# Optimization experiments

Hardware: AMD Instinct MI355X
Metric: run time of the kernel (lower is better)

## Reference

```python
import jax, jax.numpy as jnp
import numpy as np

GEMMA2_TANH_SCALE = 50.0
N_HEADS = 16
HEAD_DIM = 128
NEG_INF = -1e9


def setup_inputs() -> dict:
    key = jax.random.key(0)
    ks = jax.random.split(key, 5)
    B, S, D = 2, 2048, 2048
    H, HD = N_HEADS, HEAD_DIM
    x = jax.random.normal(ks[0], (B, S, D), jnp.float32)
    w_scale = 1.0 / np.sqrt(D)
    wq = jax.random.normal(ks[1], (H * HD, D), jnp.float32) * w_scale
    wk = jax.random.normal(ks[2], (H * HD, D), jnp.float32) * w_scale
    wv = jax.random.normal(ks[3], (H * HD, D), jnp.float32) * w_scale
    wo = jax.random.normal(ks[4], (D, H * HD), jnp.float32) * w_scale
    # RoPE frequencies: standard llama theta=10000, [S, HD/2, (cos,sin)]
    inv_freq = 1.0 / (10000.0 ** (np.arange(0, HD, 2, dtype=np.float32) / HD))
    ang = np.outer(np.arange(S, dtype=np.float32), inv_freq)  # [S, HD/2]
    freqs_cis = jnp.asarray(np.stack([np.cos(ang), np.sin(ang)], axis=-1), jnp.float32)
    # causal additive mask [1,1,S,S]
    causal = np.tril(np.ones((S, S), dtype=bool))
    mask = jnp.asarray(np.where(causal, 0.0, NEG_INF).astype(np.float32))[None, None]
    return {"x": x, "freqs_cis": freqs_cis, "mask": mask,
            "wq": wq, "wk": wk, "wv": wv, "wo": wo}


def _apply_rope(t, freqs_cis):
    # t: [B,S,H,HD]; treat adjacent pairs as complex, multiply by e^{i*ang}
    B, S, H, HD = t.shape
    tr = t.reshape(B, S, H, HD // 2, 2)
    a, b = tr[..., 0], tr[..., 1]
    cos = freqs_cis[None, :, None, :, 0]
    sin = freqs_cis[None, :, None, :, 1]
    out = jnp.stack([a * cos - b * sin, a * sin + b * cos], axis=-1)
    return out.reshape(B, S, H, HD)


def reference(x, freqs_cis, mask, wq, wk, wv, wo):
    B, S, D = x.shape
    H, HD = N_HEADS, HEAD_DIM
    xq = (x @ wq.T).reshape(B, S, H, HD)
    xk = (x @ wk.T).reshape(B, S, H, HD)
    xv = (x @ wv.T).reshape(B, S, H, HD)
    q = _apply_rope(xq, freqs_cis).transpose(0, 2, 1, 3)  # [B,H,S,HD]
    k = _apply_rope(xk, freqs_cis).transpose(0, 2, 1, 3)
    v = xv.transpose(0, 2, 1, 3)
    scores = jnp.einsum('bhqd,bhkd->bhqk', q, k) / np.sqrt(HD).astype(np.float32)
    # gemma2 tanh softcap
    scores = jnp.tanh(scores / GEMMA2_TANH_SCALE) * GEMMA2_TANH_SCALE
    scores = scores + mask
    probs = jax.nn.softmax(scores.astype(jnp.float32), axis=-1).astype(q.dtype)
    out = jnp.einsum('bhqk,bhkd->bhqd', probs, v)
    out = out.transpose(0, 2, 1, 3).reshape(B, S, H * HD)
    return out @ wo.T
```

## Files before the change

### kernel.cpp

```cpp
#include <hip/hip_runtime.h>
#include <hip/hip_bf16.h>
#include <stdint.h>

#define DEVI __device__ __forceinline__

typedef __attribute__((ext_vector_type(8))) short bf16x8;
typedef __attribute__((ext_vector_type(4))) short bf16x4;
typedef __attribute__((ext_vector_type(4))) float f32x4;

static constexpr int S_  = 2048;
static constexpr int H_  = 16;
static constexpr int HD_ = 128;

DEVI short f2bf(float f){
  uint32_t u = __builtin_bit_cast(uint32_t, f);
  u += 0x7fffu + ((u >> 16) & 1u);
  return (short)(u >> 16);
}
DEVI float bf2f(short s){
  uint32_t u = ((uint32_t)(uint16_t)s) << 16;
  return __builtin_bit_cast(float, u);
}

DEVI void gll16(const short* g, const short* lds_base){
  __builtin_amdgcn_global_load_lds(
      (const __attribute__((address_space(1))) void*)g,
      (__attribute__((address_space(3))) void*)lds_base,
      16, 0, 0);
}

__global__ __launch_bounds__(256)
void cvt6_kernel(const float* __restrict__ x,  const float* __restrict__ wq,
                 const float* __restrict__ wk, const float* __restrict__ wv,
                 const float* __restrict__ wo,
                 short* __restrict__ XB, short* __restrict__ WQKV, short* __restrict__ WO)
{
  const float* src; short* dst;
  switch (blockIdx.y){
    case 0:  src = x;           dst = XB;             break;
    case 1:  src = x + 4194304; dst = XB + 4194304;   break;
    case 2:  src = wq;          dst = WQKV;           break;
    case 3:  src = wk;          dst = WQKV + 4194304; break;
    case 4:  src = wv;          dst = WQKV + 8388608; break;
    default: src = wo;          dst = WO;             break;
  }
  int i = blockIdx.x * 256 + threadIdx.x;
  float4 v = ((const float4*)src)[i];
  bf16x4 o;
  o[0] = f2bf(v.x); o[1] = f2bf(v.y); o[2] = f2bf(v.z); o[3] = f2bf(v.w);
  ((bf16x4*)dst)[i] = o;
}

template<int EPI>
__global__ __launch_bounds__(256)
void gemm_bt(const short* __restrict__ A, const short* __restrict__ Bw,
             float* __restrict__ Cout, short* __restrict__ Qo,
             short* __restrict__ Ko, short* __restrict__ Vo,
             int M, int N, int K)
{
  __shared__ short As[128*32];
  __shared__ short Bs[128*32];
  int tiles_m = M >> 7;
  int bm = (int)blockIdx.x % tiles_m;
  int bn = (int)blockIdx.x / tiles_m;
  int tid = threadIdx.x;
  int w = tid >> 6, l = tid & 63;
  int l15 = l & 15, lg = l >> 4;
  int wr = w >> 1, wc = w & 1;

  f32x4 acc[4][4];
#pragma unroll
  for (int i = 0; i < 4; ++i)
#pragma unroll
    for (int j = 0; j < 4; ++j) acc[i][j] = 0;

  for (int k0 = 0; k0 < K; k0 += 32){
#pragma unroll
    for (int j = 0; j < 2; ++j){
      int c = j*256 + w*64 + l;
      int row = c >> 2, kc = c & 3;
      gll16(A  + ((size_t)(bm*128 + row))*K + k0 + kc*8, As + (j*256 + w*64)*8);
      gll16(Bw + ((size_t)(bn*128 + row))*K + k0 + kc*8, Bs + (j*256 + w*64)*8);
    }
    __syncthreads();
    bf16x8 af[4], bfv[4];
#pragma unroll
    for (int i = 0; i < 4; ++i){
      af[i]  = *(const bf16x8*)(As + (wr*64 + i*16 + l15)*32 + lg*8);
      bfv[i] = *(const bf16x8*)(Bs + (wc*64 + i*16 + l15)*32 + lg*8);
    }
#pragma unroll
    for (int i = 0; i < 4; ++i)
#pragma unroll
      for (int j = 0; j < 4; ++j)
        acc[i][j] = __builtin_amdgcn_mfma_f32_16x16x32_bf16(af[i], bfv[j], acc[i][j], 0, 0, 0);
    __syncthreads();
  }

#pragma unroll
  for (int i = 0; i < 4; ++i){
#pragma unroll
    for (int j = 0; j < 4; ++j){
      int m0 = bm*128 + wr*64 + i*16 + lg*4;
      int n  = bn*128 + wc*64 + j*16 + l15;
      if (EPI == 0){
#pragma unroll
        for (int r = 0; r < 4; ++r)
          Cout[(size_t)(m0 + r)*N + n] = acc[i][j][r];
      } else {
        int sect = n >> 11;
        int nn = n & 2047;
        int h = nn >> 7, d = nn & 127;
        if (sect == 2){
          int b = m0 >> 11, s = m0 & 2047;
          bf16x4 pv;
#pragma unroll
          for (int r = 0; r < 4; ++r) pv[r] = f2bf(acc[i][j][r]);
          *(bf16x4*)(Vo + (((size_t)(b*H_ + h))*HD_ + d)*S_ + s) = pv;
        } else {
          short* dst = (sect == 0) ? Qo : Ko;
#pragma unroll
          for (int r = 0; r < 4; ++r){
            int m = m0 + r; int b = m >> 11, s = m & 2047;
            dst[(((size_t)(b*H_ + h))*S_ + s)*HD_ + d] = f2bf(acc[i][j][r]);
          }
        }
      }
    }
  }
}

__global__ __launch_bounds__(256)
void rope_kernel(short* __restrict__ q, short* __restrict__ k,
                 const float* __restrict__ fr){
  int idx = blockIdx.x * 256 + threadIdx.x;
  short* p = (blockIdx.y == 0) ? q : k;
  int t = idx & 15, row = idx >> 4;
  int s = row & (S_ - 1);
  short* ptr = p + (size_t)row*HD_ + t*8;
  bf16x8 v = *(bf16x8*)ptr;
  const float* f = fr + ((size_t)s*64 + t*4)*2;
  float4 f0 = *(const float4*)f;
  float4 f1 = *(const float4*)(f + 4);
  bf16x8 o;
  float a, b;
  a = bf2f(v[0]); b = bf2f(v[1]); o[0] = f2bf(a*f0.x - b*f0.y); o[1] = f2bf(a*f0.y + b*f0.x);
  a = bf2f(v[2]); b = bf2f(v[3]); o[2] = f2bf(a*f0.z - b*f0.w); o[3] = f2bf(a*f0.w + b*f0.z);
  a = bf2f(v[4]); b = bf2f(v[5]); o[4] = f2bf(a*f1.x - b*f1.y); o[5] = f2bf(a*f1.y + b*f1.x);
  a = bf2f(v[6]); b = bf2f(v[7]); o[6] = f2bf(a*f1.z - b*f1.w); o[7] = f2bf(a*f1.w + b*f1.z);
  *(bf16x8*)ptr = o;
}

__global__ __launch_bounds__(256)
void attn_kernel(const short* __restrict__ Q, const short* __restrict__ Kg,
                 const short* __restrict__ Vt, short* __restrict__ Ob)
{
  __shared__ short Ks[64*136];
  __shared__ short Vs[128*72];
  __shared__ short Ps[4][16*72];
  int bx = blockIdx.x, bh = blockIdx.y;
  int tid = threadIdx.x;
  int w = tid >> 6, l = tid & 63, l15 = l & 15, lg = l >> 4;
  int b = bh >> 4, h = bh & 15;
  const float LOG2E = 1.4426950408889634f;

  for (int pass = 0; pass < 2; ++pass){
    int qt = pass ? (31 - bx) : bx;
    int q0 = qt*64 + w*16;

    bf16x8 qf[4];
    {
      const short* qp = Q + ((size_t)bh*S_ + q0 + l15)*HD_ + lg*8;
#pragma unroll
      for (int kc = 0; kc < 4; ++kc) qf[kc] = *(const bf16x8*)(qp + kc*32);
    }
    f32x4 o[8];
#pragma unroll
    for (int dt = 0; dt < 8; ++dt) o[dt] = 0;
    float mrow[4], lrow[4];
#pragma unroll
    for (int r = 0; r < 4; ++r){ mrow[r] = -1e30f; lrow[r] = 0.f; }

    for (int kt = 0; kt <= qt; ++kt){
      int kv0 = kt*64;
      __syncthreads();
#pragma unroll
      for (int j = 0; j < 4; ++j){
        int c = tid + j*256; int row = c >> 4, k8 = c & 15;
        *(bf16x8*)(Ks + row*136 + k8*8) =
          *(const bf16x8*)(Kg + ((size_t)bh*S_ + kv0 + row)*HD_ + k8*8);
      }
#pragma unroll
      for (int j = 0; j < 4; ++j){
        int c = tid + j*256; int d = c >> 3, k8 = c & 7;
        *(bf16x8*)(Vs + d*72 + k8*8) =
          *(const bf16x8*)(Vt + ((size_t)bh*HD_ + d)*S_ + kv0 + k8*8);
      }
      __syncthreads();

      f32x4 sa[4];
#pragma unroll
      for (int tj = 0; tj < 4; ++tj) sa[tj] = 0;
#pragma unroll
      for (int tj = 0; tj < 4; ++tj)
#pragma unroll
        for (int kc = 0; kc < 4; ++kc){
          bf16x8 kf = *(const bf16x8*)(Ks + (tj*16 + l15)*136 + kc*32 + lg*8);
          sa[tj] = __builtin_amdgcn_mfma_f32_16x16x32_bf16(qf[kc], kf, sa[tj], 0, 0, 0);
        }

#pragma unroll
      for (int tj = 0; tj < 4; ++tj)
#pragma unroll
        for (int r = 0; r < 4; ++r){
          float sc = sa[tj][r] * 0.08838834764831845f;
          float y = sc * 0.02f;
          float ay = fabsf(y);
          float e = exp2f(ay * (-2.0f * LOG2E));
          float th = __fdividef(1.0f - e, 1.0f + e);
          th = (y < 0.f) ? -th : th;
          sc = 50.0f * th;
          if (kt == qt){
            int kcol = kv0 + tj*16 + l15;
            int qrow = q0 + lg*4 + r;
            if (kcol > qrow) sc = -1e9f;
          }
          sa[tj][r] = sc;
        }

#pragma unroll
      for (int r = 0; r < 4; ++r){
        float tm = fmaxf(fmaxf(sa[0][r], sa[1][r]), fmaxf(sa[2][r], sa[3][r]));
#pragma unroll
        for (int off = 1; off < 16; off <<= 1) tm = fmaxf(tm, __shfl_xor(tm, off, 64));
        float mn = fmaxf(mrow[r], tm);
        float scl = exp2f((mrow[r] - mn) * LOG2E);
        mrow[r] = mn;
        lrow[r] *= scl;
#pragma unroll
        for (int dt = 0; dt < 8; ++dt) o[dt][r] *= scl;
        float ts = 0.f;
#pragma unroll
        for (int tj = 0; tj < 4; ++tj){
          float p = exp2f((sa[tj][r] - mn) * LOG2E);
          sa[tj][r] = p;
          ts += p;
        }
#pragma unroll
        for (int off = 1; off < 16; off <<= 1) ts += __shfl_xor(ts, off, 64);
        lrow[r] += ts;
      }

      short* ps = &Ps[w][0];
#pragma unroll
      for (int tj = 0; tj < 4; ++tj)
#pragma unroll
        for (int r = 0; r < 4; ++r)
          ps[(lg*4 + r)*72 + tj*16 + l15] = f2bf(sa[tj][r]);
      bf16x8 pa0 = *(const bf16x8*)(ps + l15*72 + lg*8);
      bf16x8 pa1 = *(const bf16x8*)(ps + l15*72 + 32 + lg*8);

#pragma unroll
      for (int dt = 0; dt < 8; ++dt){
        bf16x8 v0 = *(const bf16x8*)(Vs + (dt*16 + l15)*72 + lg*8);
        bf16x8 v1 = *(const bf16x8*)(Vs + (dt*16 + l15)*72 + 32 + lg*8);
        o[dt] = __builtin_amdgcn_mfma_f32_16x16x32_bf16(pa0, v0, o[dt], 0, 0, 0);
        o[dt] = __builtin_amdgcn_mfma_f32_16x16x32_bf16(pa1, v1, o[dt], 0, 0, 0);
      }
    }

    float inv[4];
#pragma unroll
    for (int r = 0; r < 4; ++r) inv[r] = __fdividef(1.0f, lrow[r]);
#pragma unroll
    for (int dt = 0; dt < 8; ++dt)
#pragma unroll
      for (int r = 0; r < 4; ++r){
        int qrow = q0 + lg*4 + r;
        Ob[((size_t)(b*S_ + qrow))*(H_*HD_) + h*HD_ + dt*16 + l15] = f2bf(o[dt][r] * inv[r]);
      }
  }
}

extern "C" void kernel_launch(void* const* d_in, const int* in_sizes, int n_in,
                              void* d_out, int out_size, void* d_ws, size_t ws_size,
                              hipStream_t stream)
{
  const float* x  = (const float*)d_in[0];
  const float* fr = (const float*)d_in[1];
  const float* wq = (const float*)d_in[3];
  const float* wk = (const float*)d_in[4];
  const float* wv = (const float*)d_in[5];
  const float* wo = (const float*)d_in[6];
  float* out = (float*)d_out;

  char* ws = (char*)d_ws;
  short* XB   = (short*)(ws + 0);
  short* WQKV = (short*)(ws + 16777216);
  short* WO   = (short*)(ws + 41943040);
  short* QB   = (short*)(ws + 50331648);
  short* KB   = (short*)(ws + 67108864);
  short* VT   = (short*)(ws + 83886080);
  short* AB   = (short*)(ws + 0);

  cvt6_kernel<<<dim3(4096, 6), 256, 0, stream>>>(x, wq, wk, wv, wo, XB, WQKV, WO);
  gemm_bt<1><<<dim3(32*48), 256, 0, stream>>>(XB, WQKV, nullptr, QB, KB, VT, 4096, 6144, 2048);
  rope_kernel<<<dim3(4096, 2), 256, 0, stream>>>(QB, KB, fr);
  attn_kernel<<<dim3(16, 32), 256, 0, stream>>>(QB, KB, VT, AB);
  gemm_bt<0><<<dim3(32*16), 256, 0, stream>>>(AB, WO, out, nullptr, nullptr, nullptr, 4096, 2048, 2048);
}
```

Baseline: 494.3 us.

## Use fixed softcap max to drop online softmax rescaling in attention

Because the tanh softcap bounds every score by 50, the kernel now uses a constant max of 50 instead of a running row max. That removes the per-tile max reduction, the rescaling of the accumulators and the per-tile sum shuffles, and folds tanh and exp into a single sigmoid-style expression. Row sums are kept per lane and reduced once at the end. The P tile in LDS also gets an XOR swizzle to reduce bank conflicts. The risk is precision: subtracting a fixed max of 50 can push small probabilities toward underflow, but fp32 exp with a bounded range should stay accurate.

```diff
diff --git a/kernel.cpp b/kernel.cpp
--- a/kernel.cpp
+++ b/kernel.cpp
@@ -162,7 +162,7 @@
   int tid = threadIdx.x;
   int w = tid >> 6, l = tid & 63, l15 = l & 15, lg = l >> 4;
   int b = bh >> 4, h = bh & 15;
-  const float LOG2E = 1.4426950408889634f;
+  const float C1 = 0.0051007025f;
 
   for (int pass = 0; pass < 2; ++pass){
     int qt = pass ? (31 - bx) : bx;
@@ -177,9 +177,9 @@
     f32x4 o[8];
 #pragma unroll
     for (int dt = 0; dt < 8; ++dt) o[dt] = 0;
-    float mrow[4], lrow[4];
-#pragma unroll
-    for (int r = 0; r < 4; ++r){ mrow[r] = -1e30f; lrow[r] = 0.f; }
+    float lp[4];
+#pragma unroll
+    for (int r = 0; r < 4; ++r) lp[r] = 0.f;
 
     for (int kt = 0; kt <= qt; ++kt){
       int kv0 = kt*64;
@@ -213,52 +213,29 @@
       for (int tj = 0; tj < 4; ++tj)
 #pragma unroll
         for (int r = 0; r < 4; ++r){
-          float sc = sa[tj][r] * 0.08838834764831845f;
-          float y = sc * 0.02f;
-          float ay = fabsf(y);
-          float e = exp2f(ay * (-2.0f * LOG2E));
-          float th = __fdividef(1.0f - e, 1.0f + e);
-          th = (y < 0.f) ? -th : th;
-          sc = 50.0f * th;
+          float e1 = exp2f(sa[tj][r] * C1) + 1.0f;
+          float rc = __fdividef(144.269504f, e1);
+          float p  = exp2f(72.134752f - rc);
           if (kt == qt){
             int kcol = kv0 + tj*16 + l15;
             int qrow = q0 + lg*4 + r;
-            if (kcol > qrow) sc = -1e9f;
+            if (kcol > qrow) p = 0.f;
           }
-          sa[tj][r] = sc;
-        }
-
-#pragma unroll
-      for (int r = 0; r < 4; ++r){
-        float tm = fmaxf(fmaxf(sa[0][r], sa[1][r]), fmaxf(sa[2][r], sa[3][r]));
-#pragma unroll
-        for (int off = 1; off < 16; off <<= 1) tm = fmaxf(tm, __shfl_xor(tm, off, 64));
-        float mn = fmaxf(mrow[r], tm);
-        float scl = exp2f((mrow[r] - mn) * LOG2E);
-        mrow[r] = mn;
-        lrow[r] *= scl;
-#pragma unroll
-        for (int dt = 0; dt < 8; ++dt) o[dt][r] *= scl;
-        float ts = 0.f;
-#pragma unroll
-        for (int tj = 0; tj < 4; ++tj){
-          float p = exp2f((sa[tj][r] - mn) * LOG2E);
+          lp[r] += p;
           sa[tj][r] = p;
-          ts += p;
-        }
-#pragma unroll
-        for (int off = 1; off < 16; off <<= 1) ts += __shfl_xor(ts, off, 64);
-        lrow[r] += ts;
-      }
+        }
 
       short* ps = &Ps[w][0];
 #pragma unroll
       for (int tj = 0; tj < 4; ++tj)
 #pragma unroll
-        for (int r = 0; r < 4; ++r)
-          ps[(lg*4 + r)*72 + tj*16 + l15] = f2bf(sa[tj][r]);
-      bf16x8 pa0 = *(const bf16x8*)(ps + l15*72 + lg*8);
-      bf16x8 pa1 = *(const bf16x8*)(ps + l15*72 + 32 + lg*8);
+        for (int r = 0; r < 4; ++r){
+          int row = lg*4 + r;
+          int col = tj*16 + l15;
+          ps[row*72 + (col ^ ((row & 8) << 1))] = f2bf(sa[tj][r]);
+        }
+      bf16x8 pa0 = *(const bf16x8*)(ps + l15*72 + ((lg*8)      ^ ((l15 & 8) << 1)));
+      bf16x8 pa1 = *(const bf16x8*)(ps + l15*72 + ((32 + lg*8) ^ ((l15 & 8) << 1)));
 
 #pragma unroll
       for (int dt = 0; dt < 8; ++dt){
@@ -271,7 +248,12 @@
 
     float inv[4];
 #pragma unroll
-    for (int r = 0; r < 4; ++r) inv[r] = __fdividef(1.0f, lrow[r]);
+    for (int r = 0; r < 4; ++r){
+      float ts = lp[r];
+#pragma unroll
+      for (int off = 1; off < 16; off <<= 1) ts += __shfl_xor(ts, off, 64);
+      inv[r] = __fdividef(1.0f, ts);
+    }
 #pragma unroll
     for (int dt = 0; dt < 8; ++dt)
 #pragma unroll
```

Result: no change. 499.5 us (+1.0%).
